# Kernel tuning notes

Hardware: AMD Instinct MI355X
Metric: run time of the kernel (lower is better)

Reference implementation:

```python
import jax, jax.numpy as jnp
import numpy as np

N, L, D, H, MLP_MULT = 2, 384, 512, 8, 4
HD = D // H
DM = D * MLP_MULT
EPS = 1e-5


def _linear_params(key, out_dim, in_dim, scale=0.02):
    kw, kb = jax.random.split(key)
    w = jax.random.normal(kw, (out_dim, in_dim), jnp.float32) * scale
    b = jax.random.normal(kb, (out_dim,), jnp.float32) * scale
    return w, b


def setup_inputs() -> dict:
    key = jax.random.key(0)
    ks = jax.random.split(key, 12)
    x = jax.random.normal(ks[0], (N, L, D), jnp.float32)
    mem = jax.random.normal(ks[1], (N, L, D), jnp.float32)
    pairwise_distances = jax.random.normal(ks[2], (N, L, L, D), jnp.float32)
    mem_padding_mask = jax.random.randint(ks[3], (N, L), 0, 2).astype(bool)
    qw, qb = _linear_params(ks[4], D, D)
    kvw, kvb = _linear_params(ks[5], 2 * D, D)
    pw, pb = _linear_params(ks[6], D, D)
    edw, edb = _linear_params(ks[7], H, D)
    w1, b1 = _linear_params(ks[8], DM, D)
    w2, b2 = _linear_params(ks[9], DM, DM)
    w3, b3 = _linear_params(ks[10], D, DM)
    return {
        'x': x, 'mem': mem, 'pairwise_distances': pairwise_distances,
        'mem_padding_mask': mem_padding_mask,
        'qw': qw, 'qb': qb, 'kvw': kvw, 'kvb': kvb, 'pw': pw, 'pb': pb,
        'edw': edw, 'edb': edb,
        'ln1_g': jnp.ones((D,), jnp.float32), 'ln1_b': jnp.zeros((D,), jnp.float32),
        'ln2_g': jnp.ones((D,), jnp.float32), 'ln2_b': jnp.zeros((D,), jnp.float32),
        'w1': w1, 'b1': b1, 'w2': w2, 'b2': b2, 'w3': w3, 'b3': b3,
    }


def _layernorm(x, g, b):
    m = jnp.mean(x, axis=-1, keepdims=True)
    v = jnp.mean((x - m) ** 2, axis=-1, keepdims=True)
    return (x - m) * jax.lax.rsqrt(v + EPS) * g + b


def reference(x, mem, pairwise_distances, mem_padding_mask,
              qw, qb, kvw, kvb, pw, pb, edw, edb,
              ln1_g, ln1_b, ln2_g, ln2_b,
              w1, b1, w2, b2, w3, b3):
    scale = HD ** -0.5
    a_in = _layernorm(x, ln1_g, ln1_b)
    a_mem = _layernorm(mem, ln1_g, ln1_b)

    q = (a_in @ qw.T + qb).reshape(N, L, H, HD).transpose(0, 2, 1, 3)   # (N,H,L1,HD)
    kv = (a_mem @ kvw.T + kvb).reshape(N, L, 2, H, HD)
    k = kv[:, :, 0].transpose(0, 2, 1, 3)                               # (N,H,L2,HD)
    v = kv[:, :, 1].transpose(0, 2, 1, 3)

    scores = jnp.einsum('bhid,bhjd->bhij', q, k) * scale                # (N,H,L1,L2)

    # T5-style relative position bias from pairwise distances
    bias = (pairwise_distances @ edw.T + edb)                            # (N,L1,L2,H)
    scores = scores + bias.transpose(0, 3, 1, 2)

    # padding mask (True = padded); rows that are fully padded get a zero
    # mask instead (then their output is zeroed after attention)
    all_pad = jnp.all(mem_padding_mask, axis=-1)                         # (N,)
    neg_inf = jnp.asarray(-jnp.inf, scores.dtype)
    mask = jnp.where(mem_padding_mask[:, None, None, :], neg_inf, 0.0)
    mask = jnp.where(all_pad[:, None, None, None], 0.0, mask)
    scores = scores + mask

    attn = jax.nn.softmax(scores, axis=-1)
    out = jnp.einsum('bhij,bhjd->bhid', attn, v)                         # (N,H,L1,HD)
    out = out * (~all_pad)[:, None, None, None]
    out = out.transpose(0, 2, 1, 3).reshape(N, L, D)

    x = x + (out @ pw.T + pb)

    h = _layernorm(x, ln2_g, ln2_b)
    h = jax.nn.silu(h @ w1.T + b1)
    h = jax.nn.silu(h @ w2.T + b2)
    h = h @ w3.T + b3
    return x + h
```

## Files before the change

kernel.cpp:

```cpp
#include <hip/hip_runtime.h>
#include <hip/hip_bf16.h>
#include <math.h>

#define NB   2
#define LSEQ 384
#define DMODEL 512
#define NH   8
#define HD2  64
#define DMLP 2048
#define LL2  (LSEQ*LSEQ)
#define ROWS (NB*LSEQ)

using bf16x8 = __attribute__((ext_vector_type(8))) short;
using f32x4  = __attribute__((ext_vector_type(4))) float;

__device__ __forceinline__ unsigned short f2bf(float f) {
    union { __hip_bfloat16 h; unsigned short u; } cv;
    cv.h = __float2bfloat16(f);
    return cv.u;
}

__device__ __forceinline__ void gload_lds16(const void* g, void* l) {
    __builtin_amdgcn_global_load_lds(
        (const __attribute__((address_space(1))) void*)g,
        (__attribute__((address_space(3))) void*)l, 16, 0, 0);
}

__device__ __forceinline__ void wait_vmcnt(int rem) {
    if (rem >= 3)      asm volatile("s_waitcnt vmcnt(12)" ::: "memory");
    else if (rem == 2) asm volatile("s_waitcnt vmcnt(8)"  ::: "memory");
    else if (rem == 1) asm volatile("s_waitcnt vmcnt(4)"  ::: "memory");
    else               asm volatile("s_waitcnt vmcnt(0)"  ::: "memory");
}

__global__ __launch_bounds__(256) void cvt_all_kernel(
        const float* __restrict__ s0, const float* __restrict__ s1,
        const float* __restrict__ s2, const float* __restrict__ s3,
        const float* __restrict__ s4, const float* __restrict__ s5,
        const float* __restrict__ edw,
        unsigned short* __restrict__ d0, unsigned short* __restrict__ d1,
        unsigned short* __restrict__ d2, unsigned short* __restrict__ d3,
        unsigned short* __restrict__ d4, unsigned short* __restrict__ d5,
        unsigned short* __restrict__ edwb) {
    const int stride = gridDim.x * blockDim.x;
    const int t0 = blockIdx.x * blockDim.x + threadIdx.x;
    const float* srcs[6] = {s0, s1, s2, s3, s4, s5};
    unsigned short* dsts[6] = {d0, d1, d2, d3, d4, d5};
    const int nf4[6] = {DMODEL*DMODEL/4, 2*DMODEL*DMODEL/4, DMODEL*DMODEL/4,
                        DMLP*DMODEL/4, DMLP*DMLP/4, DMLP*DMODEL/4};
    #pragma unroll
    for (int a = 0; a < 6; a++) {
        const float* s = srcs[a];
        unsigned short* d = dsts[a];
        for (int i = t0; i < nf4[a]; i += stride) {
            float4 v = *(const float4*)(s + (size_t)i * 4);
            ushort4 o = {f2bf(v.x), f2bf(v.y), f2bf(v.z), f2bf(v.w)};
            *(ushort4*)(d + (size_t)i * 4) = o;
        }
    }
    for (int i = t0; i < 16 * 512 / 4; i += stride) {
        int row = (i * 4) >> 9;
        float4 v = {0.f, 0.f, 0.f, 0.f};
        if (row < 8) v = *(const float4*)(edw + (size_t)i * 4);
        ushort4 o = {f2bf(v.x), f2bf(v.y), f2bf(v.z), f2bf(v.w)};
        *(ushort4*)(edwb + (size_t)i * 4) = o;
    }
}

__global__ __launch_bounds__(256) void ln_kernel(const float* __restrict__ src0,
                                                 const float* __restrict__ src1,
                                                 const float* __restrict__ g,
                                                 const float* __restrict__ b,
                                                 unsigned short* __restrict__ dst0,
                                                 unsigned short* __restrict__ dst1) {
    int lane = threadIdx.x & 63;
    int row  = blockIdx.x * 4 + (threadIdx.x >> 6);
    const float* src = (row < ROWS) ? src0 : src1;
    unsigned short* dst = (row < ROWS) ? dst0 : dst1;
    int r2 = (row < ROWS) ? row : row - ROWS;
    const float* p = src + (size_t)r2 * DMODEL + lane * 8;
    float4 v0 = *(const float4*)p;
    float4 v1 = *(const float4*)(p + 4);
    float s  = v0.x + v0.y + v0.z + v0.w + v1.x + v1.y + v1.z + v1.w;
    float ss = v0.x*v0.x + v0.y*v0.y + v0.z*v0.z + v0.w*v0.w
             + v1.x*v1.x + v1.y*v1.y + v1.z*v1.z + v1.w*v1.w;
    #pragma unroll
    for (int o = 32; o; o >>= 1) { s += __shfl_xor(s, o); ss += __shfl_xor(ss, o); }
    float m   = s * (1.0f / DMODEL);
    float var = ss * (1.0f / DMODEL) - m * m;
    float r   = rsqrtf(var + 1e-5f);
    float4 g0 = *(const float4*)(g + lane * 8);
    float4 g1 = *(const float4*)(g + lane * 8 + 4);
    float4 b0 = *(const float4*)(b + lane * 8);
    float4 b1 = *(const float4*)(b + lane * 8 + 4);
    unsigned short* q = dst + (size_t)r2 * DMODEL + lane * 8;
    ushort4 lo = {f2bf((v0.x - m) * r * g0.x + b0.x), f2bf((v0.y - m) * r * g0.y + b0.y),
                  f2bf((v0.z - m) * r * g0.z + b0.z), f2bf((v0.w - m) * r * g0.w + b0.w)};
    ushort4 hi = {f2bf((v1.x - m) * r * g1.x + b1.x), f2bf((v1.y - m) * r * g1.y + b1.y),
                  f2bf((v1.z - m) * r * g1.z + b1.z), f2bf((v1.w - m) * r * g1.w + b1.w)};
    *(ushort4*)q = lo;
    *(ushort4*)(q + 4) = hi;
}

__global__ __launch_bounds__(256) void bias_mfma(const float* __restrict__ pd,
                                                 const unsigned short* __restrict__ edwb,
                                                 const float* __restrict__ edb,
                                                 const int* __restrict__ mask,
                                                 float* __restrict__ biasb) {
    __shared__ float Asb[2][64 * 64];
    const int tid = threadIdx.x;
    const int lane = tid & 63, w = tid >> 6;
    const int T = blockIdx.x;
    const size_t row0 = (size_t)T * 64;
    const int n = T / 2304;
    const int rem64 = (T - n * 2304) * 64;
    const int i = rem64 / LSEQ, j0 = rem64 % LSEQ;

    int pad = 1;
    for (int j = lane; j < LSEQ; j += 64) pad &= (mask[n * LSEQ + j] != 0) ? 1 : 0;
    unsigned long long bal = __ballot(pad);
    const int ap = (bal == ~0ull) ? 1 : 0;

    int rr[4], sc[4];
    #pragma unroll
    for (int q = 0; q < 4; q++) {
        int s = q * 256 + tid;
        rr[q] = s >> 4;
        int cs = s & 15;
        sc[q] = (cs & 8) | ((cs & 7) ^ (rr[q] & 7));
    }

    const int c = lane & 15, g = lane >> 4;
    f32x4 acc = {};

    #pragma unroll
    for (int q = 0; q < 4; q++)
        gload_lds16(pd + (row0 + rr[q]) * DMODEL + sc[q] * 4, &Asb[0][(q * 256 + tid) * 4]);
    __syncthreads();

    for (int kc = 0; kc < 8; kc++) {
        if (kc < 7) {
            const int nb = (kc + 1) & 1;
            #pragma unroll
            for (int q = 0; q < 4; q++)
                gload_lds16(pd + (row0 + rr[q]) * DMODEL + (kc + 1) * 64 + sc[q] * 4,
                            &Asb[nb][(q * 256 + tid) * 4]);
        }
        const float* Ab = &Asb[kc & 1][0];
        #pragma unroll
        for (int ks = 0; ks < 2; ks++) {
            const int ch0 = (8 * ks) | ((2 * g) ^ (c & 7));
            const int ch1 = (8 * ks) | ((2 * g + 1) ^ (c & 7));
            float4 a0 = *(const float4*)&Ab[(w * 16 + c) * 64 + ch0 * 4];
            float4 a1 = *(const float4*)&Ab[(w * 16 + c) * 64 + ch1 * 4];
            bf16x8 af;
            af[0] = (short)f2bf(a0.x); af[1] = (short)f2bf(a0.y);
            af[2] = (short)f2bf(a0.z); af[3] = (short)f2bf(a0.w);
            af[4] = (short)f2bf(a1.x); af[5] = (short)f2bf(a1.y);
            af[6] = (short)f2bf(a1.z); af[7] = (short)f2bf(a1.w);
            bf16x8 bfv = *(const bf16x8*)&edwb[c * 512 + kc * 64 + ks * 32 + g * 8];
            acc = __builtin_amdgcn_mfma_f32_16x16x32_bf16(af, bfv, acc, 0, 0, 0);
        }
        if (kc < 7) __syncthreads();
    }

    if (c < 8) {
        const float eb = edb[c];
        const int jj = j0 + w * 16 + g * 4;
        int4 mv = *(const int4*)&mask[n * LSEQ + jj];
        const float NEGINF = -__builtin_inff();
        float4 o;
        o.x = acc[0] + eb + ((!ap && mv.x) ? NEGINF : 0.0f);
        o.y = acc[1] + eb + ((!ap && mv.y) ? NEGINF : 0.0f);
        o.z = acc[2] + eb + ((!ap && mv.z) ? NEGINF : 0.0f);
        o.w = acc[3] + eb + ((!ap && mv.w) ? NEGINF : 0.0f);
        *(float4*)&biasb[(size_t)(n * 8 + c) * LL2 + (size_t)i * LSEQ + jj] = o;
    }
}

template<int ACT, int RES, int OBF>
__device__ __forceinline__ void gemm_body(const unsigned short* __restrict__ A,
        const unsigned short* __restrict__ W, const float* __restrict__ bv,
        const float* __restrict__ Rsd, void* __restrict__ Cv,
        int Nn, int K, int m0, int n0, short* As, short* Ws) {
    const int tid  = threadIdx.x;
    const int lane = tid & 63, w = tid >> 6;
    const int wr = w >> 1, wc = w & 1;
    const int s0 = tid, s1 = 256 + tid;
    const int r0 = s0 >> 3, c0 = ((s0 & 7) ^ (r0 & 7)) << 3;
    const int r1 = s1 >> 3, c1 = ((s1 & 7) ^ (r1 & 7)) << 3;
    const unsigned short* ag0 = A + (size_t)(m0 + r0) * K + c0;
    const unsigned short* ag1 = A + (size_t)(m0 + r1) * K + c1;
    const unsigned short* wg0 = W + (size_t)(n0 + r0) * K + c0;
    const unsigned short* wg1 = W + (size_t)(n0 + r1) * K + c1;

    f32x4 acc[2][2] = {};
    const int lc = lane & 15, lr = lane >> 4;
    const int KT = K >> 6;

    #pragma unroll
    for (int t = 0; t < 4; t++) {
        const int b = t * 4096, k0 = t << 6;
        gload_lds16(ag0 + k0, &As[b + s0 * 8]);
        gload_lds16(ag1 + k0, &As[b + s1 * 8]);
        gload_lds16(wg0 + k0, &Ws[b + s0 * 8]);
        gload_lds16(wg1 + k0, &Ws[b + s1 * 8]);
    }

    for (int t = 0; t < KT; t++) {
        int rem = KT - 1 - t; if (rem > 3) rem = 3;
        wait_vmcnt(rem);
        __builtin_amdgcn_s_barrier();
        __builtin_amdgcn_sched_barrier(0);
        const int cur = (t & 3) * 4096;
        bf16x8 af[2][2], bfr[2][2];
        #pragma unroll
        for (int m = 0; m < 2; m++) {
            const int rra = wr * 32 + m * 16 + lc;
            #pragma unroll
            for (int kk = 0; kk < 2; kk++) {
                const int cc = (lr + kk * 4) ^ (rra & 7);
                af[m][kk] = *(const bf16x8*)&As[cur + rra * 64 + cc * 8];
            }
        }
        #pragma unroll
        for (int nn = 0; nn < 2; nn++) {
            const int rrb = wc * 32 + nn * 16 + lc;
            #pragma unroll
            for (int kk = 0; kk < 2; kk++) {
                const int cc = (lr + kk * 4) ^ (rrb & 7);
                bfr[nn][kk] = *(const bf16x8*)&Ws[cur + rrb * 64 + cc * 8];
            }
        }
        #pragma unroll
        for (int m = 0; m < 2; m++)
            #pragma unroll
            for (int nn = 0; nn < 2; nn++) {
                acc[m][nn] = __builtin_amdgcn_mfma_f32_16x16x32_bf16(af[m][0], bfr[nn][0], acc[m][nn], 0, 0, 0);
                acc[m][nn] = __builtin_amdgcn_mfma_f32_16x16x32_bf16(af[m][1], bfr[nn][1], acc[m][nn], 0, 0, 0);
            }
        if (t + 4 < KT) {
            __builtin_amdgcn_sched_barrier(0);
            __builtin_amdgcn_s_barrier();
            const int b = cur, k0 = (t + 4) << 6;
            gload_lds16(ag0 + k0, &As[b + s0 * 8]);
            gload_lds16(ag1 + k0, &As[b + s1 * 8]);
            gload_lds16(wg0 + k0, &Ws[b + s0 * 8]);
            gload_lds16(wg1 + k0, &Ws[b + s1 * 8]);
        }
    }

    #pragma unroll
    for (int nn = 0; nn < 2; nn++) {
        int gcol = n0 + wc * 32 + nn * 16 + lc;
        float bb = bv[gcol];
        #pragma unroll
        for (int m = 0; m < 2; m++) {
            #pragma unroll
            for (int r = 0; r < 4; r++) {
                int grow = m0 + wr * 32 + m * 16 + lr * 4 + r;
                float o = acc[m][nn][r] + bb;
                if (ACT) o = o / (1.0f + expf(-o));
                if (RES) o += Rsd[(size_t)grow * Nn + gcol];
                if (OBF) ((unsigned short*)Cv)[(size_t)grow * Nn + gcol] = f2bf(o);
                else     ((float*)Cv)[(size_t)grow * Nn + gcol] = o;
            }
        }
    }
}

template<int ACT, int RES, int OBF>
__global__ __launch_bounds__(256) void mfma_gemm(const unsigned short* __restrict__ A,
                                                 const unsigned short* __restrict__ W,
                                                 const float* __restrict__ bv,
                                                 const float* __restrict__ Rsd,
                                                 void* __restrict__ Cv, int Nn, int K) {
    __shared__ short As[4 * 4096];
    __shared__ short Ws[4 * 4096];
    gemm_body<ACT, RES, OBF>(A, W, bv, Rsd, Cv, Nn, K, blockIdx.y * 64, blockIdx.x * 64, As, Ws);
}

__global__ __launch_bounds__(256) void qkv_gemm(const unsigned short* __restrict__ a_in,
                                                const unsigned short* __restrict__ a_mem,
                                                const unsigned short* __restrict__ qwb,
                                                const unsigned short* __restrict__ kvwb,
                                                const float* __restrict__ qbv,
                                                const float* __restrict__ kvbv,
                                                float* __restrict__ qbuf,
                                                float* __restrict__ kvbuf) {
    __shared__ short As[4 * 4096];
    __shared__ short Ws[4 * 4096];
    const int bx = blockIdx.x;
    const unsigned short* A; const unsigned short* W; const float* bv; float* C; int Nn, n0;
    if (bx < 8) { A = a_in;  W = qwb;  bv = qbv;  C = qbuf;  Nn = DMODEL;     n0 = bx * 64; }
    else        { A = a_mem; W = kvwb; bv = kvbv; C = kvbuf; Nn = 2 * DMODEL; n0 = (bx - 8) * 64; }
    gemm_body<0, 0, 0>(A, W, bv, nullptr, C, Nn, DMODEL, blockIdx.y * 64, n0, As, Ws);
}

__global__ __launch_bounds__(256) void scores_kernel(const float* __restrict__ q,
                                                     const float* __restrict__ kv,
                                                     const float* __restrict__ biasb,
                                                     float* __restrict__ S) {
    const int n = blockIdx.z, h = blockIdx.y;
    const int it = blockIdx.x / 12, jt = blockIdx.x % 12;
    __shared__ float Qs[64][32];
    __shared__ float Ks[64][32];
    const int tid = threadIdx.x;
    const int r = tid >> 3, c = (tid & 7) << 3;
    {
        const float* qp = q + ((size_t)(n * LSEQ + it * 32 + r)) * DMODEL + h * HD2 + c;
        float4 q0 = *(const float4*)qp;
        float4 q1 = *(const float4*)(qp + 4);
        Qs[c+0][r]=q0.x; Qs[c+1][r]=q0.y; Qs[c+2][r]=q0.z; Qs[c+3][r]=q0.w;
        Qs[c+4][r]=q1.x; Qs[c+5][r]=q1.y; Qs[c+6][r]=q1.z; Qs[c+7][r]=q1.w;
        const float* kp = kv + ((size_t)(n * LSEQ + jt * 32 + r)) * (2 * DMODEL) + h * HD2 + c;
        float4 k0 = *(const float4*)kp;
        float4 k1 = *(const float4*)(kp + 4);
        Ks[c+0][r]=k0.x; Ks[c+1][r]=k0.y; Ks[c+2][r]=k0.z; Ks[c+3][r]=k0.w;
        Ks[c+4][r]=k1.x; Ks[c+5][r]=k1.y; Ks[c+6][r]=k1.z; Ks[c+7][r]=k1.w;
    }
    __syncthreads();
    const int tx = tid & 15, ty = tid >> 4;
    float acc[2][2] = {{0.f,0.f},{0.f,0.f}};
    #pragma unroll
    for (int k = 0; k < 64; k++) {
        float2 a  = *(const float2*)&Qs[k][ty << 1];
        float2 b2 = *(const float2*)&Ks[k][tx << 1];
        acc[0][0] = fmaf(a.x, b2.x, acc[0][0]);
        acc[0][1] = fmaf(a.x, b2.y, acc[0][1]);
        acc[1][0] = fmaf(a.y, b2.x, acc[1][0]);
        acc[1][1] = fmaf(a.y, b2.y, acc[1][1]);
    }
    #pragma unroll
    for (int i2 = 0; i2 < 2; i2++) {
        int gi = it * 32 + (ty << 1) + i2;
        #pragma unroll
        for (int j2 = 0; j2 < 2; j2++) {
            int gj = jt * 32 + (tx << 1) + j2;
            size_t idx = ((size_t)(n * 8 + h)) * LL2 + (size_t)gi * LSEQ + gj;
            S[idx] = acc[i2][j2] * 0.125f + biasb[idx];
        }
    }
}

__global__ __launch_bounds__(256) void softmax_kernel(float* __restrict__ S) {
    int lane = threadIdx.x & 63;
    int row  = blockIdx.x * 4 + (threadIdx.x >> 6);
    float* p = S + (size_t)row * LSEQ;
    float v[6];
    #pragma unroll
    for (int cc = 0; cc < 6; cc++) v[cc] = p[cc * 64 + lane];
    float mx = v[0];
    #pragma unroll
    for (int cc = 1; cc < 6; cc++) mx = fmaxf(mx, v[cc]);
    #pragma unroll
    for (int o = 32; o; o >>= 1) mx = fmaxf(mx, __shfl_xor(mx, o));
    float sum = 0.f;
    #pragma unroll
    for (int cc = 0; cc < 6; cc++) { v[cc] = expf(v[cc] - mx); sum += v[cc]; }
    #pragma unroll
    for (int o = 32; o; o >>= 1) sum += __shfl_xor(sum, o);
    float inv = 1.0f / sum;
    #pragma unroll
    for (int cc = 0; cc < 6; cc++) p[cc * 64 + lane] = v[cc] * inv;
}

__global__ __launch_bounds__(256) void av_kernel(const float* __restrict__ S,
                                                 const float* __restrict__ kv,
                                                 const int* __restrict__ mask,
                                                 unsigned short* __restrict__ outb) {
    const int it = blockIdx.x, h = blockIdx.y, n = blockIdx.z;
    __shared__ float Ps[32][68];
    __shared__ float Vs[64][68];
    const int tid = threadIdx.x;
    const int lane = tid & 63;
    int pad = 1;
    for (int j = lane; j < LSEQ; j += 64) pad &= (mask[n * LSEQ + j] != 0) ? 1 : 0;
    unsigned long long bal = __ballot(pad != 0);
    const float zf = (bal == 0xFFFFFFFFFFFFFFFFull) ? 0.0f : 1.0f;
    const int tx = tid & 15, ty = tid >> 4;
    const int pr = tid >> 3, pc = (tid & 7) << 3;
    const int vr = tid >> 2, vc = (tid & 3) << 4;
    float acc0[4] = {0,0,0,0}, acc1[4] = {0,0,0,0};
    for (int j0 = 0; j0 < LSEQ; j0 += 64) {
        const float* sp = S + ((size_t)(n * 8 + h)) * LL2 + (size_t)(it * 32 + pr) * LSEQ + j0 + pc;
        float4 p0 = *(const float4*)sp;
        float4 p1 = *(const float4*)(sp + 4);
        *(float4*)&Ps[pr][pc]     = p0;
        *(float4*)&Ps[pr][pc + 4] = p1;
        #pragma unroll
        for (int u = 0; u < 4; u++) {
            float4 vvv = *(const float4*)&kv[((size_t)(n * LSEQ + j0 + vr)) * (2 * DMODEL)
                                             + DMODEL + h * HD2 + vc + 4 * u];
            *(float4*)&Vs[vr][vc + 4 * u] = vvv;
        }
        __syncthreads();
        #pragma unroll
        for (int j = 0; j < 64; j++) {
            float pa  = Ps[ty][j];
            float pb2 = Ps[ty + 16][j];
            float4 vv = *(const float4*)&Vs[j][tx << 2];
            acc0[0] = fmaf(pa,  vv.x, acc0[0]);
            acc0[1] = fmaf(pa,  vv.y, acc0[1]);
            acc0[2] = fmaf(pa,  vv.z, acc0[2]);
            acc0[3] = fmaf(pa,  vv.w, acc0[3]);
            acc1[0] = fmaf(pb2, vv.x, acc1[0]);
            acc1[1] = fmaf(pb2, vv.y, acc1[1]);
            acc1[2] = fmaf(pb2, vv.z, acc1[2]);
            acc1[3] = fmaf(pb2, vv.w, acc1[3]);
        }
        __syncthreads();
    }
    int i0 = it * 32;
    ushort4 o0 = {f2bf(acc0[0]*zf), f2bf(acc0[1]*zf), f2bf(acc0[2]*zf), f2bf(acc0[3]*zf)};
    ushort4 o1 = {f2bf(acc1[0]*zf), f2bf(acc1[1]*zf), f2bf(acc1[2]*zf), f2bf(acc1[3]*zf)};
    *(ushort4*)&outb[((size_t)(n * LSEQ + i0 + ty)) * DMODEL + h * HD2 + (tx << 2)]      = o0;
    *(ushort4*)&outb[((size_t)(n * LSEQ + i0 + ty + 16)) * DMODEL + h * HD2 + (tx << 2)] = o1;
}

extern "C" void kernel_launch(void* const* d_in, const int* in_sizes, int n_in,
                              void* d_out, int out_size, void* d_ws, size_t ws_size,
                              hipStream_t stream) {
    const float* x    = (const float*)d_in[0];
    const float* mem  = (const float*)d_in[1];
    const float* pd   = (const float*)d_in[2];
    const int*   mask = (const int*)d_in[3];
    const float* qw   = (const float*)d_in[4];
    const float* qbv  = (const float*)d_in[5];
    const float* kvw  = (const float*)d_in[6];
    const float* kvbv = (const float*)d_in[7];
    const float* pw   = (const float*)d_in[8];
    const float* pbv  = (const float*)d_in[9];
    const float* edw  = (const float*)d_in[10];
    const float* edb  = (const float*)d_in[11];
    const float* ln1g = (const float*)d_in[12];
    const float* ln1b = (const float*)d_in[13];
    const float* ln2g = (const float*)d_in[14];
    const float* ln2b = (const float*)d_in[15];
    const float* w1   = (const float*)d_in[16];
    const float* b1   = (const float*)d_in[17];
    const float* w2   = (const float*)d_in[18];
    const float* b2   = (const float*)d_in[19];
    const float* w3   = (const float*)d_in[20];
    const float* b3   = (const float*)d_in[21];

    float* wsf = (float*)d_ws;
    float* biasb  = wsf + 16;
    float* scores = biasb + (size_t)NB * NH * LL2;
    float* qbuf   = scores + (size_t)NB * NH * LL2;
    float* kvbuf  = qbuf + (size_t)ROWS * DMODEL;
    float* x1buf  = kvbuf + (size_t)ROWS * 2 * DMODEL;
    unsigned short* a_in  = (unsigned short*)(x1buf + (size_t)ROWS * DMODEL);
    unsigned short* a_mem = a_in  + (size_t)ROWS * DMODEL;
    unsigned short* attno = a_mem + (size_t)ROWS * DMODEL;
    unsigned short* h0    = attno + (size_t)ROWS * DMODEL;
    unsigned short* h1    = h0    + (size_t)ROWS * DMODEL;
    unsigned short* h2    = h1    + (size_t)ROWS * DMLP;
    unsigned short* qwb   = h2    + (size_t)ROWS * DMLP;
    unsigned short* kvwb  = qwb   + (size_t)DMODEL * DMODEL;
    unsigned short* pwb   = kvwb  + (size_t)2 * DMODEL * DMODEL;
    unsigned short* w1b   = pwb   + (size_t)DMODEL * DMODEL;
    unsigned short* w2b   = w1b   + (size_t)DMLP * DMODEL;
    unsigned short* w3b   = w2b   + (size_t)DMLP * DMLP;
    unsigned short* edwb  = w3b   + (size_t)DMLP * DMODEL;

    float* outp = (float*)d_out;

    cvt_all_kernel<<<2048, 256, 0, stream>>>(qw, kvw, pw, w1, w2, w3, edw,
                                             qwb, kvwb, pwb, w1b, w2b, w3b, edwb);
    ln_kernel<<<2 * ROWS / 4, 256, 0, stream>>>(x, mem, ln1g, ln1b, a_in, a_mem);
    bias_mfma<<<NB * LL2 / 64, 256, 0, stream>>>(pd, edwb, edb, mask, biasb);

    qkv_gemm<<<dim3(24, 12), 256, 0, stream>>>(a_in, a_mem, qwb, kvwb, qbv, kvbv, qbuf, kvbuf);

    scores_kernel<<<dim3(144, NH, NB), 256, 0, stream>>>(qbuf, kvbuf, biasb, scores);
    softmax_kernel<<<(NB * NH * LSEQ) / 4, 256, 0, stream>>>(scores);
    av_kernel<<<dim3(12, NH, NB), 256, 0, stream>>>(scores, kvbuf, mask, attno);

    mfma_gemm<0,1,0><<<dim3(DMODEL/64, ROWS/64), 256, 0, stream>>>(attno, pwb, pbv, x, x1buf, DMODEL, DMODEL);
    ln_kernel<<<ROWS / 4, 256, 0, stream>>>(x1buf, x1buf, ln2g, ln2b, h0, h0);
    mfma_gemm<1,0,1><<<dim3(DMLP/64, ROWS/64), 256, 0, stream>>>(h0, w1b, b1, nullptr, h1, DMLP, DMODEL);
    mfma_gemm<1,0,1><<<dim3(DMLP/64, ROWS/64), 256, 0, stream>>>(h1, w2b, b2, nullptr, h2, DMLP, DMLP);
    mfma_gemm<0,1,0><<<dim3(DMODEL/64, ROWS/64), 256, 0, stream>>>(h2, w3b, b3, x1buf, outp, DMODEL, DMLP);
}
```

Baseline: 264.2 us.

## Merge LN1 into weight-convert kernel, triple-buffer bias loads, preload edw fragments

Folds the first layernorm into the weight conversion kernel so one launch does both, using the first 384 blocks for LN and the rest for conversion. The bias MFMA kernel moves to a three-stage LDS ring with explicit vmcnt waits and one barrier per step, and keeps the edw B fragments in registers instead of reloading them each iteration. Softmax switches to fast __expf. Together these target launch overhead and load latency in the pairwise-distance bias pass, at the cost of more LDS and registers per block.

```diff
diff --git a/kernel.cpp b/kernel.cpp
--- a/kernel.cpp
+++ b/kernel.cpp
@@ -26,14 +26,10 @@
         (__attribute__((address_space(3))) void*)l, 16, 0, 0);
 }
 
-__device__ __forceinline__ void wait_vmcnt(int rem) {
-    if (rem >= 3)      asm volatile("s_waitcnt vmcnt(12)" ::: "memory");
-    else if (rem == 2) asm volatile("s_waitcnt vmcnt(8)"  ::: "memory");
-    else if (rem == 1) asm volatile("s_waitcnt vmcnt(4)"  ::: "memory");
-    else               asm volatile("s_waitcnt vmcnt(0)"  ::: "memory");
-}
-
-__global__ __launch_bounds__(256) void cvt_all_kernel(
+__global__ __launch_bounds__(256) void pre_kernel(
+        const float* __restrict__ x, const float* __restrict__ mem,
+        const float* __restrict__ ln1g, const float* __restrict__ ln1b,
+        unsigned short* __restrict__ a_in, unsigned short* __restrict__ a_mem,
         const float* __restrict__ s0, const float* __restrict__ s1,
         const float* __restrict__ s2, const float* __restrict__ s3,
         const float* __restrict__ s4, const float* __restrict__ s5,
@@ -42,8 +38,39 @@
         unsigned short* __restrict__ d2, unsigned short* __restrict__ d3,
         unsigned short* __restrict__ d4, unsigned short* __restrict__ d5,
         unsigned short* __restrict__ edwb) {
-    const int stride = gridDim.x * blockDim.x;
-    const int t0 = blockIdx.x * blockDim.x + threadIdx.x;
+    const int tid = threadIdx.x;
+    if (blockIdx.x < 384) {
+        int lane = tid & 63;
+        int row  = blockIdx.x * 4 + (tid >> 6);
+        const float* src = (row < ROWS) ? x : mem;
+        unsigned short* dst = (row < ROWS) ? a_in : a_mem;
+        int r2 = (row < ROWS) ? row : row - ROWS;
+        const float* p = src + (size_t)r2 * DMODEL + lane * 8;
+        float4 v0 = *(const float4*)p;
+        float4 v1 = *(const float4*)(p + 4);
+        float s  = v0.x + v0.y + v0.z + v0.w + v1.x + v1.y + v1.z + v1.w;
+        float ss = v0.x*v0.x + v0.y*v0.y + v0.z*v0.z + v0.w*v0.w
+                 + v1.x*v1.x + v1.y*v1.y + v1.z*v1.z + v1.w*v1.w;
+        #pragma unroll
+        for (int o = 32; o; o >>= 1) { s += __shfl_xor(s, o); ss += __shfl_xor(ss, o); }
+        float m   = s * (1.0f / DMODEL);
+        float var = ss * (1.0f / DMODEL) - m * m;
+        float r   = rsqrtf(var + 1e-5f);
+        float4 g0 = *(const float4*)(ln1g + lane * 8);
+        float4 g1 = *(const float4*)(ln1g + lane * 8 + 4);
+        float4 b0 = *(const float4*)(ln1b + lane * 8);
+        float4 b1 = *(const float4*)(ln1b + lane * 8 + 4);
+        unsigned short* q = dst + (size_t)r2 * DMODEL + lane * 8;
+        ushort4 lo = {f2bf((v0.x-m)*r*g0.x+b0.x), f2bf((v0.y-m)*r*g0.y+b0.y),
+                      f2bf((v0.z-m)*r*g0.z+b0.z), f2bf((v0.w-m)*r*g0.w+b0.w)};
+        ushort4 hi = {f2bf((v1.x-m)*r*g1.x+b1.x), f2bf((v1.y-m)*r*g1.y+b1.y),
+                      f2bf((v1.z-m)*r*g1.z+b1.z), f2bf((v1.w-m)*r*g1.w+b1.w)};
+        *(ushort4*)q = lo;
+        *(ushort4*)(q + 4) = hi;
+        return;
+    }
+    const int stride = (gridDim.x - 384) * 256;
+    const int t0 = (blockIdx.x - 384) * 256 + tid;
     const float* srcs[6] = {s0, s1, s2, s3, s4, s5};
     unsigned short* dsts[6] = {d0, d1, d2, d3, d4, d5};
     const int nf4[6] = {DMODEL*DMODEL/4, 2*DMODEL*DMODEL/4, DMODEL*DMODEL/4,
@@ -59,7 +86,7 @@
         }
     }
     for (int i = t0; i < 16 * 512 / 4; i += stride) {
-        int row = (i * 4) >> 9;
+        int row = i >> 7;
         float4 v = {0.f, 0.f, 0.f, 0.f};
         if (row < 8) v = *(const float4*)(edw + (size_t)i * 4);
         ushort4 o = {f2bf(v.x), f2bf(v.y), f2bf(v.z), f2bf(v.w)};
@@ -68,17 +95,12 @@
 }
 
 __global__ __launch_bounds__(256) void ln_kernel(const float* __restrict__ src0,
-                                                 const float* __restrict__ src1,
                                                  const float* __restrict__ g,
                                                  const float* __restrict__ b,
-                                                 unsigned short* __restrict__ dst0,
-                                                 unsigned short* __restrict__ dst1) {
+                                                 unsigned short* __restrict__ dst0) {
     int lane = threadIdx.x & 63;
     int row  = blockIdx.x * 4 + (threadIdx.x >> 6);
-    const float* src = (row < ROWS) ? src0 : src1;
-    unsigned short* dst = (row < ROWS) ? dst0 : dst1;
-    int r2 = (row < ROWS) ? row : row - ROWS;
-    const float* p = src + (size_t)r2 * DMODEL + lane * 8;
+    const float* p = src0 + (size_t)row * DMODEL + lane * 8;
     float4 v0 = *(const float4*)p;
     float4 v1 = *(const float4*)(p + 4);
     float s  = v0.x + v0.y + v0.z + v0.w + v1.x + v1.y + v1.z + v1.w;
@@ -93,11 +115,11 @@
     float4 g1 = *(const float4*)(g + lane * 8 + 4);
     float4 b0 = *(const float4*)(b + lane * 8);
     float4 b1 = *(const float4*)(b + lane * 8 + 4);
-    unsigned short* q = dst + (size_t)r2 * DMODEL + lane * 8;
-    ushort4 lo = {f2bf((v0.x - m) * r * g0.x + b0.x), f2bf((v0.y - m) * r * g0.y + b0.y),
-                  f2bf((v0.z - m) * r * g0.z + b0.z), f2bf((v0.w - m) * r * g0.w + b0.w)};
-    ushort4 hi = {f2bf((v1.x - m) * r * g1.x + b1.x), f2bf((v1.y - m) * r * g1.y + b1.y),
-                  f2bf((v1.z - m) * r * g1.z + b1.z), f2bf((v1.w - m) * r * g1.w + b1.w)};
+    unsigned short* q = dst0 + (size_t)row * DMODEL + lane * 8;
+    ushort4 lo = {f2bf((v0.x-m)*r*g0.x+b0.x), f2bf((v0.y-m)*r*g0.y+b0.y),
+                  f2bf((v0.z-m)*r*g0.z+b0.z), f2bf((v0.w-m)*r*g0.w+b0.w)};
+    ushort4 hi = {f2bf((v1.x-m)*r*g1.x+b1.x), f2bf((v1.y-m)*r*g1.y+b1.y),
+                  f2bf((v1.z-m)*r*g1.z+b1.z), f2bf((v1.w-m)*r*g1.w+b1.w)};
     *(ushort4*)q = lo;
     *(ushort4*)(q + 4) = hi;
 }
@@ -107,7 +129,7 @@
                                                  const float* __restrict__ edb,
                                                  const int* __restrict__ mask,
                                                  float* __restrict__ biasb) {
-    __shared__ float Asb[2][64 * 64];
+    __shared__ float Asb[3][64 * 64];
     const int tid = threadIdx.x;
     const int lane = tid & 63, w = tid >> 6;
     const int T = blockIdx.x;
@@ -116,6 +138,14 @@
     const int rem64 = (T - n * 2304) * 64;
     const int i = rem64 / LSEQ, j0 = rem64 % LSEQ;
 
+    const int c = lane & 15, g = lane >> 4;
+    bf16x8 bfv[8][2];
+    #pragma unroll
+    for (int kc = 0; kc < 8; kc++)
+        #pragma unroll
+        for (int ks = 0; ks < 2; ks++)
+            bfv[kc][ks] = *(const bf16x8*)&edwb[c * 512 + kc * 64 + ks * 32 + g * 8];
+
     int pad = 1;
     for (int j = lane; j < LSEQ; j += 64) pad &= (mask[n * LSEQ + j] != 0) ? 1 : 0;
     unsigned long long bal = __ballot(pad);
@@ -130,23 +160,29 @@
         sc[q] = (cs & 8) | ((cs & 7) ^ (rr[q] & 7));
     }
 
-    const int c = lane & 15, g = lane >> 4;
     f32x4 acc = {};
 
     #pragma unroll
     for (int q = 0; q < 4; q++)
         gload_lds16(pd + (row0 + rr[q]) * DMODEL + sc[q] * 4, &Asb[0][(q * 256 + tid) * 4]);
-    __syncthreads();
-
+    #pragma unroll
+    for (int q = 0; q < 4; q++)
+        gload_lds16(pd + (row0 + rr[q]) * DMODEL + 64 + sc[q] * 4, &Asb[1][(q * 256 + tid) * 4]);
+
+    #pragma unroll
     for (int kc = 0; kc < 8; kc++) {
-        if (kc < 7) {
-            const int nb = (kc + 1) & 1;
+        if (kc < 7) asm volatile("s_waitcnt vmcnt(4)" ::: "memory");
+        else        asm volatile("s_waitcnt vmcnt(0)" ::: "memory");
+        __builtin_amdgcn_s_barrier();
+        __builtin_amdgcn_sched_barrier(0);
+        if (kc + 2 < 8) {
+            const int nb = (kc + 2) % 3;
             #pragma unroll
             for (int q = 0; q < 4; q++)
-                gload_lds16(pd + (row0 + rr[q]) * DMODEL + (kc + 1) * 64 + sc[q] * 4,
+                gload_lds16(pd + (row0 + rr[q]) * DMODEL + (kc + 2) * 64 + sc[q] * 4,
                             &Asb[nb][(q * 256 + tid) * 4]);
         }
-        const float* Ab = &Asb[kc & 1][0];
+        const float* Ab = &Asb[kc % 3][0];
         #pragma unroll
         for (int ks = 0; ks < 2; ks++) {
             const int ch0 = (8 * ks) | ((2 * g) ^ (c & 7));
@@ -158,10 +194,8 @@
             af[2] = (short)f2bf(a0.z); af[3] = (short)f2bf(a0.w);
             af[4] = (short)f2bf(a1.x); af[5] = (short)f2bf(a1.y);
             af[6] = (short)f2bf(a1.z); af[7] = (short)f2bf(a1.w);
-            bf16x8 bfv = *(const bf16x8*)&edwb[c * 512 + kc * 64 + ks * 32 + g * 8];
-            acc = __builtin_amdgcn_mfma_f32_16x16x32_bf16(af, bfv, acc, 0, 0, 0);
-        }
-        if (kc < 7) __syncthreads();
+            acc = __builtin_amdgcn_mfma_f32_16x16x32_bf16(af, bfv[kc][ks], acc, 0, 0, 0);
+        }
     }
 
     if (c < 8) {
@@ -209,7 +243,10 @@
 
     for (int t = 0; t < KT; t++) {
         int rem = KT - 1 - t; if (rem > 3) rem = 3;
-        wait_vmcnt(rem);
+        if (rem >= 3)      asm volatile("s_waitcnt vmcnt(12)" ::: "memory");
+        else if (rem == 2) asm volatile("s_waitcnt vmcnt(8)"  ::: "memory");
+        else if (rem == 1) asm volatile("s_waitcnt vmcnt(4)"  ::: "memory");
+        else               asm volatile("s_waitcnt vmcnt(0)"  ::: "memory");
         __builtin_amdgcn_s_barrier();
         __builtin_amdgcn_sched_barrier(0);
         const int cur = (t & 3) * 4096;
@@ -357,7 +394,7 @@
     for (int o = 32; o; o >>= 1) mx = fmaxf(mx, __shfl_xor(mx, o));
     float sum = 0.f;
     #pragma unroll
-    for (int cc = 0; cc < 6; cc++) { v[cc] = expf(v[cc] - mx); sum += v[cc]; }
+    for (int cc = 0; cc < 6; cc++) { v[cc] = __expf(v[cc] - mx); sum += v[cc]; }
     #pragma unroll
     for (int o = 32; o; o >>= 1) sum += __shfl_xor(sum, o);
     float inv = 1.0f / sum;
@@ -466,20 +503,19 @@
 
     float* outp = (float*)d_out;
 
-    cvt_all_kernel<<<2048, 256, 0, stream>>>(qw, kvw, pw, w1, w2, w3, edw,
-                                             qwb, kvwb, pwb, w1b, w2b, w3b, edwb);
-    ln_kernel<<<2 * ROWS / 4, 256, 0, stream>>>(x, mem, ln1g, ln1b, a_in, a_mem);
+    pre_kernel<<<2048, 256, 0, stream>>>(x, mem, ln1g, ln1b, a_in, a_mem,
+                                         qw, kvw, pw, w1, w2, w3, edw,
+                                         qwb, kvwb, pwb, w1b, w2b, w3b, edwb);
     bias_mfma<<<NB * LL2 / 64, 256, 0, stream>>>(pd, edwb, edb, mask, biasb);
-
     qkv_gemm<<<dim3(24, 12), 256, 0, stream>>>(a_in, a_mem, qwb, kvwb, qbv, kvbv, qbuf, kvbuf);
 
     scores_kernel<<<dim3(144, NH, NB), 256, 0, stream>>>(qbuf, kvbuf, biasb, scores);
     softmax_kernel<<<(NB * NH * LSEQ) / 4, 256, 0, stream>>>(scores);
     av_kernel<<<dim3(12, NH, NB), 256, 0, stream>>>(scores, kvbuf, mask, attno);
 
-    mfma_gemm<0,1,0><<<dim3(DMODEL/64, ROWS/64), 256, 0, stream>>>(attno, pwb, pbv, x, x1buf, DMODEL, DMODEL);
-    ln_kernel<<<ROWS / 4, 256, 0, stream>>>(x1buf, x1buf, ln2g, ln2b, h0, h0);
-    mfma_gemm<1,0,1><<<dim3(DMLP/64, ROWS/64), 256, 0, stream>>>(h0, w1b, b1, nullptr, h1, DMLP, DMODEL);
-    mfma_gemm<1,0,1><<<dim3(DMLP/64, ROWS/64), 256, 0, stream>>>(h1, w2b, b2, nullptr, h2, DMLP, DMLP);
-    mfma_gemm<0,1,0><<<dim3(DMODEL/64, ROWS/64), 256, 0, stream>>>(h2, w3b, b3, x1buf, outp, DMODEL, DMLP);
-}
+    mfma_gemm<0,1,0><<<dim3(8, 12), 256, 0, stream>>>(attno, pwb, pbv, x, x1buf, DMODEL, DMODEL);
+    ln_kernel<<<ROWS / 4, 256, 0, stream>>>(x1buf, ln2g, ln2b, h0);
+    mfma_gemm<1,0,1><<<dim3(32, 12), 256, 0, stream>>>(h0, w1b, b1, nullptr, h1, DMLP, DMODEL);
+    mfma_gemm<1,0,1><<<dim3(32, 12), 256, 0, stream>>>(h1, w2b, b2, nullptr, h2, DMLP, DMLP);
+    mfma_gemm<0,1,0><<<dim3(8, 12), 256, 0, stream>>>(h2, w3b, b3, x1buf, outp, DMODEL, DMLP);
+}
```

Measured after the change: 272.5 us. 1.03x slower.
